# Kernel optimization log

Hardware: AMD Instinct MI355X
Metric: run time of the kernel (lower is better)

## Reference

```python
import jax, jax.numpy as jnp
import numpy as np

T_STEPS = 50000  # number of daily timesteps
HID = 512        # hidden_size: parallel ExpHydro parameter ensembles


def _hamon_pet(temp, lday):
    # Hamon PET (mm/day): 29.8 * daylight_hours * esat(T)/(T+273.2)
    esat = 0.611 * jnp.exp(17.3 * temp / (temp + 237.3))
    return 29.8 * (lday * 24.0) * esat / (temp + 273.2)


def setup_inputs() -> dict:
    key = jax.random.key(0)
    ks = jax.random.split(key, 9)
    # forcings: precip (mm/d), mean temp (degC), day-length fraction
    prcp = jax.random.uniform(ks[0], (T_STEPS,), dtype=jnp.float32) * 20.0
    temp = jax.random.uniform(ks[1], (T_STEPS,), dtype=jnp.float32) * 30.0 - 10.0
    lday = jax.random.uniform(ks[2], (T_STEPS,), dtype=jnp.float32) * 0.3 + 0.3
    x = jnp.stack([prcp, temp, lday], axis=1)  # [T, 3]
    u = lambda k, lo, hi: jax.random.uniform(k, (HID,), dtype=jnp.float32) * (hi - lo) + lo
    f = u(ks[3], 0.01, 0.1)        # baseflow recession rate (1/mm)
    smax = u(ks[4], 100.0, 1500.0)  # max soil storage (mm)
    qmax = u(ks[5], 10.0, 50.0)     # max baseflow (mm/d)
    df = u(ks[6], 0.0, 5.0)         # degree-day melt factor (mm/d/degC)
    tmax = u(ks[7], 0.0, 3.0)       # melt threshold temp (degC)
    tmin = u(ks[8], -3.0, 0.0)      # snowfall threshold temp (degC)
    return {"x": x, "f": f, "smax": smax, "qmax": qmax, "df": df, "tmax": tmax, "tmin": tmin}


def reference(x, f, smax, qmax, df, tmax, tmin):
    prcp = x[:, 0]  # [T]
    temp = x[:, 1]
    lday = x[:, 2]
    pet = _hamon_pet(temp, lday)  # [T], only depends on forcings -> precompute

    def step(carry, inp):
        s0, s1 = carry              # snow / soil storage, each [HID]
        p, t, pe = inp              # scalar forcings, broadcast vs [HID] params
        ps = jnp.where(t <= tmin, p, 0.0)                              # snowfall
        pr = p - ps                                                     # rainfall
        melt = jnp.where(t > tmax, jnp.minimum(s0, df * (t - tmax)), 0.0)
        et = jnp.where(s1 >= smax, pe, pe * s1 / smax)                  # evapotranspiration
        qb = jnp.where(s1 >= smax, qmax, qmax * jnp.exp(-f * (smax - s1)))  # baseflow
        qs = jnp.maximum(s1 - smax, 0.0)                                # bucket spill
        s0n = jnp.maximum(s0 + ps - melt, 0.0)
        s1n = jnp.maximum(s1 + pr + melt - et - qb - qs, 0.0)
        return (s0n, s1n), qb + qs

    init = (jnp.zeros((HID,), x.dtype), jnp.zeros((HID,), x.dtype))
    _, q = jax.lax.scan(step, init, (prcp, temp, pet))
    return q  # [T, HID] streamflow per timestep per ensemble member
```

## Files before the change

kernel.cpp:

```cpp
#include <hip/hip_runtime.h>

#define T_STEPS 50000
#define HID     512
#define LBASE   512
#define CHUNKS  98
#define NPAD    (T_STEPS + 64)
#define SDMAX   (2 * LBASE)

static_assert((T_STEPS + LBASE - 1) / LBASE == CHUNKS, "chunk count");
static_assert(LBASE % 16 == 0, "16-step bodies");

#define PIN2D(a) asm volatile("" : "+v"(a.x), "+v"(a.y))

__global__ void pet_pack_kernel(const float* __restrict__ x,
                                float4* __restrict__ ptp) {
    int i = blockIdx.x * 256 + threadIdx.x;
    if (i >= NPAD) return;
    float4 v = make_float4(0.f, 0.f, 0.f, 0.f);
    if (i < T_STEPS) {
        float p  = x[3 * i + 0];
        float tt = x[3 * i + 1];
        float ld = x[3 * i + 2];
        float esat = 0.611f * __expf(17.3f * tt / (tt + 237.3f));
        float pe   = 29.8f * (ld * 24.0f) * esat / (tt + 273.2f);
        v = make_float4(p, tt, pe, 0.f);
    }
    ptp[i] = v;
}

__global__ __launch_bounds__(256)
void lindley_agg_kernel(const float4* __restrict__ ptp,
                        const float* __restrict__ df_,
                        const float* __restrict__ tmax_,
                        const float* __restrict__ tmin_,
                        double2* __restrict__ dm) {
    __shared__ float4 sd[LBASE];
    const int b     = blockIdx.x;
    const int chunk = b >> 1;
    const int h     = ((b & 1) << 8) | (int)threadIdx.x;

    const float DF = df_[h], TMX = tmax_[h], TMN = tmin_[h];
    const float ndftmx = -(DF * TMX);

    const int cL = chunk * LBASE;
    const int cE = (cL + LBASE < T_STEPS) ? (cL + LBASE) : T_STEPS;
    const int n  = cE - cL;

    for (int i = threadIdx.x; i < n; i += 256) sd[i] = ptp[cL + i];
    __syncthreads();

    double D = 0.0, M = -1.0e300;
    const int n16 = n >> 4;
    for (int it = 0; it < n16; ++it) {
        const int base = it * 16;
#pragma unroll
        for (int i = 0; i < 16; ++i) {
            const float4 v = sd[base + i];
            const float cap = fmaxf(fmaf(DF, v.y, ndftmx), 0.0f);
            const float ps  = (v.y <= TMN) ? v.x : 0.0f;
            const double d  = (double)ps - (double)cap;
            D += d;
            M = fmax(M + d, (double)ps);
        }
    }
    dm[chunk * HID + h] = make_double2(D, M);
}

__global__ __launch_bounds__(64)
void lindley_scan_kernel(const double2* __restrict__ dm,
                         float* __restrict__ s0b) {
    const int h = blockIdx.x * 64 + threadIdx.x;
    const double2* dp = dm + h;
    double xv = 0.0;
    s0b[h] = 0.0f;

#define COMP(a, c)                                                            \
    {                                                                         \
        PIN2D(a);                                                             \
        xv = fmax(xv + a.x, a.y);                                             \
        s0b[(size_t)((c) + 1) * HID + h] = (float)xv;                         \
    }

    double2 p0 = dp[0];
    double2 p1 = dp[(size_t)1 * HID];
    double2 p2 = dp[(size_t)2 * HID];
    double2 p3 = dp[(size_t)3 * HID];

    COMP(p0, 0);
    p0 = dp[(size_t)4 * HID];

    for (int j = 0; j < 24; ++j) {
        const int c = 1 + 4 * j;
        COMP(p1, c);     p1 = dp[(size_t)(c + 4) * HID];
        COMP(p2, c + 1); p2 = dp[(size_t)(c + 5) * HID];
        COMP(p3, c + 2); p3 = dp[(size_t)(c + 6) * HID];
        COMP(p0, c + 3); p0 = dp[(size_t)(c + 7) * HID];
    }
#undef COMP
}

#define STEP(P, TT, PE, QV)                                                   \
    {                                                                         \
        const float dfdt = fmaf(DF, (TT), ndftmx);                            \
        const float melt = __builtin_amdgcn_fmed3f(dfdt, s0, 0.0f);           \
        const float ps   = ((TT) <= TMN) ? (P) : 0.0f;                        \
        const float w    = melt - ps;                                         \
        s0 = s0 - w;                                                          \
        const float qs   = fmaxf(s1 - SM, 0.0f);                              \
        const float m    = fminf(s1, SM);                                     \
        const float u    = fmaf(g, s1, qc);                                   \
        const float qb   = fminf(QM, __builtin_amdgcn_exp2f(u));              \
        const float npei = (PE)*ninv_sm;                                      \
        const float A    = (s1 + ((P) + w)) - qs;                             \
        const float B    = fmaf(m, npei, A);                                  \
        s1 = fmaxf(B - qb, 0.0f);                                             \
        QV = qb + qs;                                                         \
    }

__global__ __launch_bounds__(256)
void hydro_chunk_kernel(const float4* __restrict__ ptp,
                        const float*  __restrict__ s0b,
                        const float*  __restrict__ f_,
                        const float*  __restrict__ smax_,
                        const float*  __restrict__ qmax_,
                        const float*  __restrict__ df_,
                        const float*  __restrict__ tmax_,
                        const float*  __restrict__ tmin_,
                        float*        __restrict__ q) {
    __shared__ float4 sd[SDMAX];
    const int b     = blockIdx.x;
    const int chunk = b >> 1;
    const int h     = ((b & 1) << 8) | (int)threadIdx.x;

    const float F   = f_[h];
    const float SM  = smax_[h];
    const float QM  = qmax_[h];
    const float DF  = df_[h];
    const float TMX = tmax_[h];
    const float TMN = tmin_[h];

    const float g       = F * 1.4426950408889634f;
    const float qc      = __log2f(QM) - g * SM;
    const float ninv_sm = -1.0f / SM;
    const float ndftmx  = -(DF * TMX);

    const int cL    = chunk * LBASE;
    const int cE    = (cL + LBASE < T_STEPS) ? (cL + LBASE) : T_STEPS;
    const int start = (chunk >= 1) ? (cL - LBASE) : 0;
    const int n     = cE - start;

    for (int i = threadIdx.x; i < n; i += 256) sd[i] = ptp[start + i];
    __syncthreads();

    float s0 = (chunk >= 1) ? s0b[(chunk - 1) * HID + h] : 0.0f;
    float s1 = 0.0f;

    const int nWarm16 = (cL - start) >> 4;
    for (int it = 0; it < nWarm16; ++it) {
        const int base = it * 16;
        float qv;
#pragma unroll
        for (int i = 0; i < 16; ++i) {
            const float4 v = sd[base + i];
            STEP(v.x, v.y, v.z, qv);
        }
        (void)qv;
    }

    char* qbase  = (char*)q;
    unsigned off = (unsigned)cL * 2048u + (unsigned)h * 4u;
    const int wbase = cL - start;

    const int nOut16 = (cE - cL) >> 4;
    for (int it = 0; it < nOut16; ++it) {
        const int base = wbase + it * 16;
#pragma unroll
        for (int i = 0; i < 16; ++i) {
            const float4 v = sd[base + i];
            float qv;
            STEP(v.x, v.y, v.z, qv);
            *(float*)(qbase + off + (unsigned)i * 2048u) = qv;
        }
        off += 32768u;
    }
}

__global__ __launch_bounds__(64)
void hydro_serial_kernel(const float* __restrict__ x,
                         const float* __restrict__ f_,
                         const float* __restrict__ smax_,
                         const float* __restrict__ qmax_,
                         const float* __restrict__ df_,
                         const float* __restrict__ tmax_,
                         const float* __restrict__ tmin_,
                         float* __restrict__ q) {
    const int h = blockIdx.x * 64 + threadIdx.x;
    const float F = f_[h], SM = smax_[h], QM = qmax_[h];
    const float DF = df_[h], TMX = tmax_[h], TMN = tmin_[h];
    const float g       = F * 1.4426950408889634f;
    const float qc      = __log2f(QM) - g * SM;
    const float ninv_sm = -1.0f / SM;
    const float ndftmx  = -(DF * TMX);
    float s0 = 0.f, s1 = 0.f;
    for (int t = 0; t < T_STEPS; ++t) {
        const float p  = x[3 * t + 0];
        const float tt = x[3 * t + 1];
        const float ld = x[3 * t + 2];
        const float esat = 0.611f * __expf(17.3f * tt / (tt + 237.3f));
        const float pe   = 29.8f * (ld * 24.0f) * esat / (tt + 273.2f);
        float qv;
        STEP(p, tt, pe, qv);
        q[(size_t)t * HID + h] = qv;
    }
}

extern "C" void kernel_launch(void* const* d_in, const int* in_sizes, int n_in,
                              void* d_out, int out_size, void* d_ws,
                              size_t ws_size, hipStream_t stream) {
    const float* x    = (const float*)d_in[0];
    const float* f    = (const float*)d_in[1];
    const float* smax = (const float*)d_in[2];
    const float* qmax = (const float*)d_in[3];
    const float* df   = (const float*)d_in[4];
    const float* tmax = (const float*)d_in[5];
    const float* tmin = (const float*)d_in[6];
    float* q = (float*)d_out;

    const size_t PTP_BYTES = (size_t)NPAD * sizeof(float4);
    const size_t DM_OFF    = PTP_BYTES;
    const size_t DM_BYTES  = (size_t)CHUNKS * HID * sizeof(double2);
    const size_t S0B_OFF   = DM_OFF + DM_BYTES;
    const size_t S0B_BYTES = (size_t)CHUNKS * HID * sizeof(float);
    const size_t NEED      = S0B_OFF + S0B_BYTES + 65536;

    if (ws_size >= NEED) {
        float4*  ptp = (float4*)d_ws;
        double2* dm  = (double2*)((char*)d_ws + DM_OFF);
        float*   s0b = (float*)((char*)d_ws + S0B_OFF);

        pet_pack_kernel<<<(NPAD + 255) / 256, 256, 0, stream>>>(x, ptp);
        lindley_agg_kernel<<<CHUNKS * 2, 256, 0, stream>>>(ptp, df, tmax, tmin, dm);
        lindley_scan_kernel<<<HID / 64, 64, 0, stream>>>(dm, s0b);
        hydro_chunk_kernel<<<CHUNKS * 2, 256, 0, stream>>>(
            ptp, s0b, f, smax, qmax, df, tmax, tmin, q);
    } else {
        hydro_serial_kernel<<<HID / 64, 64, 0, stream>>>(
            x, f, smax, qmax, df, tmax, tmin, q);
    }
}
```

Measured before the change: 84.58 us.

## Fuse PET packing, Lindley aggregation, scan and chunk sim into one cooperative kernel

Replaces the four-kernel pipeline with a single cooperative kernel. Each block computes PET for its chunk straight into shared memory, then computes the Lindley aggregates, and the per-chunk snow carries are scanned by two blocks between grid-wide syncs. The goal is to remove three launch gaps and the global round trip of the packed forcing array. In exchange it adds two grid.sync barriers, makes 196 blocks wait idle while 2 blocks run the serial scan, and recomputes PET for the overlapping warmup window.

```diff
diff --git a/kernel.cpp b/kernel.cpp
--- a/kernel.cpp
+++ b/kernel.cpp
@@ -1,103 +1,18 @@
 #include <hip/hip_runtime.h>
+#include <hip/hip_cooperative_groups.h>
+
+namespace cg = cooperative_groups;
 
 #define T_STEPS 50000
 #define HID     512
 #define LBASE   512
 #define CHUNKS  98
-#define NPAD    (T_STEPS + 64)
 #define SDMAX   (2 * LBASE)
 
 static_assert((T_STEPS + LBASE - 1) / LBASE == CHUNKS, "chunk count");
 static_assert(LBASE % 16 == 0, "16-step bodies");
 
 #define PIN2D(a) asm volatile("" : "+v"(a.x), "+v"(a.y))
-
-__global__ void pet_pack_kernel(const float* __restrict__ x,
-                                float4* __restrict__ ptp) {
-    int i = blockIdx.x * 256 + threadIdx.x;
-    if (i >= NPAD) return;
-    float4 v = make_float4(0.f, 0.f, 0.f, 0.f);
-    if (i < T_STEPS) {
-        float p  = x[3 * i + 0];
-        float tt = x[3 * i + 1];
-        float ld = x[3 * i + 2];
-        float esat = 0.611f * __expf(17.3f * tt / (tt + 237.3f));
-        float pe   = 29.8f * (ld * 24.0f) * esat / (tt + 273.2f);
-        v = make_float4(p, tt, pe, 0.f);
-    }
-    ptp[i] = v;
-}
-
-__global__ __launch_bounds__(256)
-void lindley_agg_kernel(const float4* __restrict__ ptp,
-                        const float* __restrict__ df_,
-                        const float* __restrict__ tmax_,
-                        const float* __restrict__ tmin_,
-                        double2* __restrict__ dm) {
-    __shared__ float4 sd[LBASE];
-    const int b     = blockIdx.x;
-    const int chunk = b >> 1;
-    const int h     = ((b & 1) << 8) | (int)threadIdx.x;
-
-    const float DF = df_[h], TMX = tmax_[h], TMN = tmin_[h];
-    const float ndftmx = -(DF * TMX);
-
-    const int cL = chunk * LBASE;
-    const int cE = (cL + LBASE < T_STEPS) ? (cL + LBASE) : T_STEPS;
-    const int n  = cE - cL;
-
-    for (int i = threadIdx.x; i < n; i += 256) sd[i] = ptp[cL + i];
-    __syncthreads();
-
-    double D = 0.0, M = -1.0e300;
-    const int n16 = n >> 4;
-    for (int it = 0; it < n16; ++it) {
-        const int base = it * 16;
-#pragma unroll
-        for (int i = 0; i < 16; ++i) {
-            const float4 v = sd[base + i];
-            const float cap = fmaxf(fmaf(DF, v.y, ndftmx), 0.0f);
-            const float ps  = (v.y <= TMN) ? v.x : 0.0f;
-            const double d  = (double)ps - (double)cap;
-            D += d;
-            M = fmax(M + d, (double)ps);
-        }
-    }
-    dm[chunk * HID + h] = make_double2(D, M);
-}
-
-__global__ __launch_bounds__(64)
-void lindley_scan_kernel(const double2* __restrict__ dm,
-                         float* __restrict__ s0b) {
-    const int h = blockIdx.x * 64 + threadIdx.x;
-    const double2* dp = dm + h;
-    double xv = 0.0;
-    s0b[h] = 0.0f;
-
-#define COMP(a, c)                                                            \
-    {                                                                         \
-        PIN2D(a);                                                             \
-        xv = fmax(xv + a.x, a.y);                                             \
-        s0b[(size_t)((c) + 1) * HID + h] = (float)xv;                         \
-    }
-
-    double2 p0 = dp[0];
-    double2 p1 = dp[(size_t)1 * HID];
-    double2 p2 = dp[(size_t)2 * HID];
-    double2 p3 = dp[(size_t)3 * HID];
-
-    COMP(p0, 0);
-    p0 = dp[(size_t)4 * HID];
-
-    for (int j = 0; j < 24; ++j) {
-        const int c = 1 + 4 * j;
-        COMP(p1, c);     p1 = dp[(size_t)(c + 4) * HID];
-        COMP(p2, c + 1); p2 = dp[(size_t)(c + 5) * HID];
-        COMP(p3, c + 2); p3 = dp[(size_t)(c + 6) * HID];
-        COMP(p0, c + 3); p0 = dp[(size_t)(c + 7) * HID];
-    }
-#undef COMP
-}
 
 #define STEP(P, TT, PE, QV)                                                   \
     {                                                                         \
@@ -118,16 +33,19 @@
     }
 
 __global__ __launch_bounds__(256)
-void hydro_chunk_kernel(const float4* __restrict__ ptp,
-                        const float*  __restrict__ s0b,
-                        const float*  __restrict__ f_,
-                        const float*  __restrict__ smax_,
-                        const float*  __restrict__ qmax_,
-                        const float*  __restrict__ df_,
-                        const float*  __restrict__ tmax_,
-                        const float*  __restrict__ tmin_,
-                        float*        __restrict__ q) {
+void hydro_fused_kernel(const float* __restrict__ x,
+                        const float* __restrict__ f_,
+                        const float* __restrict__ smax_,
+                        const float* __restrict__ qmax_,
+                        const float* __restrict__ df_,
+                        const float* __restrict__ tmax_,
+                        const float* __restrict__ tmin_,
+                        double2*     __restrict__ dm,
+                        float*       __restrict__ s0b,
+                        float*       __restrict__ q) {
     __shared__ float4 sd[SDMAX];
+    cg::grid_group grid = cg::this_grid();
+
     const int b     = blockIdx.x;
     const int chunk = b >> 1;
     const int h     = ((b & 1) << 8) | (int)threadIdx.x;
@@ -149,13 +67,69 @@
     const int start = (chunk >= 1) ? (cL - LBASE) : 0;
     const int n     = cE - start;
 
-    for (int i = threadIdx.x; i < n; i += 256) sd[i] = ptp[start + i];
+    for (int i = threadIdx.x; i < n; i += 256) {
+        const int t = start + i;
+        const float p  = x[3 * t + 0];
+        const float tt = x[3 * t + 1];
+        const float ld = x[3 * t + 2];
+        const float esat = 0.611f * __expf(17.3f * tt / (tt + 237.3f));
+        const float pe   = 29.8f * (ld * 24.0f) * esat / (tt + 273.2f);
+        sd[i] = make_float4(p, tt, pe, 0.f);
+    }
     __syncthreads();
+
+    const int wbase = cL - start;
+    {
+        double D = 0.0, M = -1.0e300;
+        const int n16 = (cE - cL) >> 4;
+        for (int it = 0; it < n16; ++it) {
+            const int base = wbase + it * 16;
+#pragma unroll
+            for (int i = 0; i < 16; ++i) {
+                const float4 v = sd[base + i];
+                const float cap = fmaxf(fmaf(DF, v.y, ndftmx), 0.0f);
+                const float ps  = (v.y <= TMN) ? v.x : 0.0f;
+                const double d  = (double)ps - (double)cap;
+                D += d;
+                M = fmax(M + d, (double)ps);
+            }
+        }
+        dm[chunk * HID + h] = make_double2(D, M);
+    }
+    grid.sync();
+
+    if (b < 2) {
+        const int h2 = (b << 8) | (int)threadIdx.x;
+        const double2* dp = dm + h2;
+        double xv = 0.0;
+        s0b[h2] = 0.0f;
+#define COMP(a, c)                                                            \
+        {                                                                     \
+            PIN2D(a);                                                         \
+            xv = fmax(xv + a.x, a.y);                                         \
+            s0b[(size_t)((c) + 1) * HID + h2] = (float)xv;                    \
+        }
+        double2 p0 = dp[0];
+        double2 p1 = dp[(size_t)1 * HID];
+        double2 p2 = dp[(size_t)2 * HID];
+        double2 p3 = dp[(size_t)3 * HID];
+        COMP(p0, 0);
+        p0 = dp[(size_t)4 * HID];
+        for (int j = 0; j < 24; ++j) {
+            const int c = 1 + 4 * j;
+            COMP(p1, c);     p1 = dp[(size_t)(c + 4) * HID];
+            COMP(p2, c + 1); p2 = dp[(size_t)(c + 5) * HID];
+            COMP(p3, c + 2); p3 = dp[(size_t)(c + 6) * HID];
+            COMP(p0, c + 3); p0 = dp[(size_t)(c + 7) * HID];
+        }
+#undef COMP
+    }
+    grid.sync();
 
     float s0 = (chunk >= 1) ? s0b[(chunk - 1) * HID + h] : 0.0f;
     float s1 = 0.0f;
 
-    const int nWarm16 = (cL - start) >> 4;
+    const int nWarm16 = wbase >> 4;
     for (int it = 0; it < nWarm16; ++it) {
         const int base = it * 16;
         float qv;
@@ -169,7 +143,6 @@
 
     char* qbase  = (char*)q;
     unsigned off = (unsigned)cL * 2048u + (unsigned)h * 4u;
-    const int wbase = cL - start;
 
     const int nOut16 = (cE - cL) >> 4;
     for (int it = 0; it < nOut16; ++it) {
@@ -226,23 +199,21 @@
     const float* tmin = (const float*)d_in[6];
     float* q = (float*)d_out;
 
-    const size_t PTP_BYTES = (size_t)NPAD * sizeof(float4);
-    const size_t DM_OFF    = PTP_BYTES;
     const size_t DM_BYTES  = (size_t)CHUNKS * HID * sizeof(double2);
-    const size_t S0B_OFF   = DM_OFF + DM_BYTES;
+    const size_t S0B_OFF   = DM_BYTES;
     const size_t S0B_BYTES = (size_t)CHUNKS * HID * sizeof(float);
     const size_t NEED      = S0B_OFF + S0B_BYTES + 65536;
 
     if (ws_size >= NEED) {
-        float4*  ptp = (float4*)d_ws;
-        double2* dm  = (double2*)((char*)d_ws + DM_OFF);
+        double2* dm  = (double2*)d_ws;
         float*   s0b = (float*)((char*)d_ws + S0B_OFF);
 
-        pet_pack_kernel<<<(NPAD + 255) / 256, 256, 0, stream>>>(x, ptp);
-        lindley_agg_kernel<<<CHUNKS * 2, 256, 0, stream>>>(ptp, df, tmax, tmin, dm);
-        lindley_scan_kernel<<<HID / 64, 64, 0, stream>>>(dm, s0b);
-        hydro_chunk_kernel<<<CHUNKS * 2, 256, 0, stream>>>(
-            ptp, s0b, f, smax, qmax, df, tmax, tmin, q);
+        void* args[] = {(void*)&x, (void*)&f, (void*)&smax, (void*)&qmax,
+                        (void*)&df, (void*)&tmax, (void*)&tmin,
+                        (void*)&dm, (void*)&s0b, (void*)&q};
+        hipLaunchCooperativeKernel((void*)hydro_fused_kernel,
+                                   dim3(CHUNKS * 2), dim3(256),
+                                   args, 0, stream);
     } else {
         hydro_serial_kernel<<<HID / 64, 64, 0, stream>>>(
             x, f, smax, qmax, df, tmax, tmin, q);
```

After: 131.9 us. +55.9%, slower.

## Shrink chunks to 128 steps with 3-chunk warmup and fuse PET into consumers

Applied to the files above, without the earlier changes.

Cuts the chunk length from 512 to 128 steps, giving 782 blocks instead of 196 so more of the GPU's compute units have work. Soil-state warmup now covers 384 steps instead of 512. The separate PET packing kernel is removed, and each block computes PET from x directly into shared memory, saving a launch and a global round trip. In exchange the Lindley scan becomes four times longer and more serial, the agg kernel runs more blocks, and the shorter soil warmup could affect accuracy if soil state has not converged.

```diff
diff --git a/kernel.cpp b/kernel.cpp
--- a/kernel.cpp
+++ b/kernel.cpp
@@ -2,34 +2,27 @@
 
 #define T_STEPS 50000
 #define HID     512
-#define LBASE   512
-#define CHUNKS  98
-#define NPAD    (T_STEPS + 64)
-#define SDMAX   (2 * LBASE)
+#define LBASE   128
+#define CHUNKS  391
+#define WARMCH  3
+#define WARM    (WARMCH * LBASE)
+#define SDMAX   (WARM + LBASE)
 
 static_assert((T_STEPS + LBASE - 1) / LBASE == CHUNKS, "chunk count");
-static_assert(LBASE % 16 == 0, "16-step bodies");
+static_assert(LBASE % 16 == 0 && WARM % 16 == 0, "16-step bodies");
+static_assert((CHUNKS - 1) == 97 * 4 + 2, "scan rotation layout");
 
 #define PIN2D(a) asm volatile("" : "+v"(a.x), "+v"(a.y))
 
-__global__ void pet_pack_kernel(const float* __restrict__ x,
-                                float4* __restrict__ ptp) {
-    int i = blockIdx.x * 256 + threadIdx.x;
-    if (i >= NPAD) return;
-    float4 v = make_float4(0.f, 0.f, 0.f, 0.f);
-    if (i < T_STEPS) {
-        float p  = x[3 * i + 0];
-        float tt = x[3 * i + 1];
-        float ld = x[3 * i + 2];
-        float esat = 0.611f * __expf(17.3f * tt / (tt + 237.3f));
-        float pe   = 29.8f * (ld * 24.0f) * esat / (tt + 273.2f);
-        v = make_float4(p, tt, pe, 0.f);
-    }
-    ptp[i] = v;
-}
+#define PET_FROM_X(t, P, TT, PE)                                              \
+    const float P  = x[3 * (t) + 0];                                          \
+    const float TT = x[3 * (t) + 1];                                          \
+    const float ld_##P = x[3 * (t) + 2];                                      \
+    const float esat_##P = 0.611f * __expf(17.3f * TT / (TT + 237.3f));       \
+    const float PE = 29.8f * (ld_##P * 24.0f) * esat_##P / (TT + 273.2f);
 
 __global__ __launch_bounds__(256)
-void lindley_agg_kernel(const float4* __restrict__ ptp,
+void lindley_agg_kernel(const float* __restrict__ x,
                         const float* __restrict__ df_,
                         const float* __restrict__ tmax_,
                         const float* __restrict__ tmin_,
@@ -46,7 +39,10 @@
     const int cE = (cL + LBASE < T_STEPS) ? (cL + LBASE) : T_STEPS;
     const int n  = cE - cL;
 
-    for (int i = threadIdx.x; i < n; i += 256) sd[i] = ptp[cL + i];
+    for (int i = threadIdx.x; i < n; i += 256) {
+        PET_FROM_X(cL + i, p, tt, pe);
+        sd[i] = make_float4(p, tt, pe, 0.f);
+    }
     __syncthreads();
 
     double D = 0.0, M = -1.0e300;
@@ -80,22 +76,24 @@
         xv = fmax(xv + a.x, a.y);                                             \
         s0b[(size_t)((c) + 1) * HID + h] = (float)xv;                         \
     }
+#define COMPS(PJ, c)                                                          \
+    { COMP(PJ, c); PJ = dp[(size_t)((c) + 4) * HID]; }
 
     double2 p0 = dp[0];
     double2 p1 = dp[(size_t)1 * HID];
     double2 p2 = dp[(size_t)2 * HID];
     double2 p3 = dp[(size_t)3 * HID];
 
-    COMP(p0, 0);
-    p0 = dp[(size_t)4 * HID];
-
-    for (int j = 0; j < 24; ++j) {
-        const int c = 1 + 4 * j;
-        COMP(p1, c);     p1 = dp[(size_t)(c + 4) * HID];
-        COMP(p2, c + 1); p2 = dp[(size_t)(c + 5) * HID];
-        COMP(p3, c + 2); p3 = dp[(size_t)(c + 6) * HID];
-        COMP(p0, c + 3); p0 = dp[(size_t)(c + 7) * HID];
-    }
+    for (int j = 0; j < 97; ++j) {
+        const int c = 4 * j;
+        COMPS(p0, c);
+        COMPS(p1, c + 1);
+        COMPS(p2, c + 2);
+        COMPS(p3, c + 3);
+    }
+    COMP(p0, 388);
+    COMP(p1, 389);
+#undef COMPS
 #undef COMP
 }
 
@@ -118,15 +116,15 @@
     }
 
 __global__ __launch_bounds__(256)
-void hydro_chunk_kernel(const float4* __restrict__ ptp,
-                        const float*  __restrict__ s0b,
-                        const float*  __restrict__ f_,
-                        const float*  __restrict__ smax_,
-                        const float*  __restrict__ qmax_,
-                        const float*  __restrict__ df_,
-                        const float*  __restrict__ tmax_,
-                        const float*  __restrict__ tmin_,
-                        float*        __restrict__ q) {
+void hydro_chunk_kernel(const float* __restrict__ x,
+                        const float* __restrict__ s0b,
+                        const float* __restrict__ f_,
+                        const float* __restrict__ smax_,
+                        const float* __restrict__ qmax_,
+                        const float* __restrict__ df_,
+                        const float* __restrict__ tmax_,
+                        const float* __restrict__ tmin_,
+                        float*       __restrict__ q) {
     __shared__ float4 sd[SDMAX];
     const int b     = blockIdx.x;
     const int chunk = b >> 1;
@@ -146,13 +144,16 @@
 
     const int cL    = chunk * LBASE;
     const int cE    = (cL + LBASE < T_STEPS) ? (cL + LBASE) : T_STEPS;
-    const int start = (chunk >= 1) ? (cL - LBASE) : 0;
+    const int start = (chunk >= WARMCH) ? (cL - WARM) : 0;
     const int n     = cE - start;
 
-    for (int i = threadIdx.x; i < n; i += 256) sd[i] = ptp[start + i];
+    for (int i = threadIdx.x; i < n; i += 256) {
+        PET_FROM_X(start + i, p, tt, pe);
+        sd[i] = make_float4(p, tt, pe, 0.f);
+    }
     __syncthreads();
 
-    float s0 = (chunk >= 1) ? s0b[(chunk - 1) * HID + h] : 0.0f;
+    float s0 = (chunk >= WARMCH) ? s0b[(chunk - WARMCH) * HID + h] : 0.0f;
     float s1 = 0.0f;
 
     const int nWarm16 = (cL - start) >> 4;
@@ -203,11 +204,7 @@
     const float ndftmx  = -(DF * TMX);
     float s0 = 0.f, s1 = 0.f;
     for (int t = 0; t < T_STEPS; ++t) {
-        const float p  = x[3 * t + 0];
-        const float tt = x[3 * t + 1];
-        const float ld = x[3 * t + 2];
-        const float esat = 0.611f * __expf(17.3f * tt / (tt + 237.3f));
-        const float pe   = 29.8f * (ld * 24.0f) * esat / (tt + 273.2f);
+        PET_FROM_X(t, p, tt, pe);
         float qv;
         STEP(p, tt, pe, qv);
         q[(size_t)t * HID + h] = qv;
@@ -226,23 +223,19 @@
     const float* tmin = (const float*)d_in[6];
     float* q = (float*)d_out;
 
-    const size_t PTP_BYTES = (size_t)NPAD * sizeof(float4);
-    const size_t DM_OFF    = PTP_BYTES;
     const size_t DM_BYTES  = (size_t)CHUNKS * HID * sizeof(double2);
-    const size_t S0B_OFF   = DM_OFF + DM_BYTES;
+    const size_t S0B_OFF   = DM_BYTES;
     const size_t S0B_BYTES = (size_t)CHUNKS * HID * sizeof(float);
     const size_t NEED      = S0B_OFF + S0B_BYTES + 65536;
 
     if (ws_size >= NEED) {
-        float4*  ptp = (float4*)d_ws;
-        double2* dm  = (double2*)((char*)d_ws + DM_OFF);
+        double2* dm  = (double2*)d_ws;
         float*   s0b = (float*)((char*)d_ws + S0B_OFF);
 
-        pet_pack_kernel<<<(NPAD + 255) / 256, 256, 0, stream>>>(x, ptp);
-        lindley_agg_kernel<<<CHUNKS * 2, 256, 0, stream>>>(ptp, df, tmax, tmin, dm);
+        lindley_agg_kernel<<<CHUNKS * 2, 256, 0, stream>>>(x, df, tmax, tmin, dm);
         lindley_scan_kernel<<<HID / 64, 64, 0, stream>>>(dm, s0b);
         hydro_chunk_kernel<<<CHUNKS * 2, 256, 0, stream>>>(
-            ptp, s0b, f, smax, qmax, df, tmax, tmin, q);
+            x, s0b, f, smax, qmax, df, tmax, tmin, q);
     } else {
         hydro_serial_kernel<<<HID / 64, 64, 0, stream>>>(
             x, f, smax, qmax, df, tmax, tmin, q);
```

Measured after the change: 113.5 us. +34.2%, slower.
